# Performance work log

Measured on AMD Instinct MI355X. Metric: run time of the kernel, lower is better.

The kernel has to match this reference:

```python
import jax, jax.numpy as jnp
import numpy as np

N_NODES = 50000
N_EDGES = 400000
IN_CH = 256
HID = 64
OUT_CH = 64
HEADS = 4
N_NTYPES = 3
N_ETYPES = 4
EDGE_DIM = 32
NEG_SLOPE = 0.2
LN_EPS = 1e-5


def _glorot(key, shape, fan_in, fan_out):
    gain = float(np.sqrt(2.0))  # calculate_gain('relu')
    limit = gain * np.sqrt(6.0 / (fan_in + fan_out))
    return jax.random.uniform(key, shape, jnp.float32, -limit, limit)


def setup_inputs() -> dict:
    key = jax.random.key(0)
    ks = jax.random.split(key, 24)
    HC1 = HEADS * HID
    inp = {
        'x': jax.random.normal(ks[0], (N_NODES, IN_CH), jnp.float32),
        'edge_index': jax.random.randint(ks[1], (2, N_EDGES), 0, N_NODES, jnp.int32),
        'node_type': jax.random.randint(ks[2], (N_NODES,), 0, N_NTYPES, jnp.int32),
        'edge_type': jax.random.randint(ks[3], (N_EDGES,), 0, N_ETYPES, jnp.int32),
        'edge_attr': jax.random.normal(ks[4], (N_EDGES, EDGE_DIM), jnp.float32),
        # layer 1 (in -> hid, concat=True)
        'W_src1': _glorot(ks[5], (N_NTYPES, IN_CH, HC1), IN_CH, HC1),
        'W_dst1': _glorot(ks[6], (N_NTYPES, IN_CH, HC1), IN_CH, HC1),
        'att_src1': _glorot(ks[7], (N_ETYPES, HEADS, HID), HEADS, HID),
        'att_dst1': _glorot(ks[8], (N_ETYPES, HEADS, HID), HEADS, HID),
        'W_edge1': _glorot(ks[9], (N_ETYPES, EDGE_DIM, HC1), EDGE_DIM, HC1),
        'att_edge1': _glorot(ks[10], (N_ETYPES, HEADS, HID), HEADS, HID),
        'bias1': jnp.zeros((HC1,), jnp.float32),
        'ln_gamma1': jnp.ones((HC1,), jnp.float32),
        'ln_beta1': jnp.zeros((HC1,), jnp.float32),
        # layer 2 (heads*hid -> out, concat=False)
        'W_src2': _glorot(ks[11], (N_NTYPES, HC1, HEADS * OUT_CH), HC1, HEADS * OUT_CH),
        'W_dst2': _glorot(ks[12], (N_NTYPES, HC1, HEADS * OUT_CH), HC1, HEADS * OUT_CH),
        'att_src2': _glorot(ks[13], (N_ETYPES, HEADS, OUT_CH), HEADS, OUT_CH),
        'att_dst2': _glorot(ks[14], (N_ETYPES, HEADS, OUT_CH), HEADS, OUT_CH),
        'W_edge2': _glorot(ks[15], (N_ETYPES, EDGE_DIM, HEADS * OUT_CH), EDGE_DIM, HEADS * OUT_CH),
        'att_edge2': _glorot(ks[16], (N_ETYPES, HEADS, OUT_CH), HEADS, OUT_CH),
        'bias2': jnp.zeros((OUT_CH,), jnp.float32),
    }
    return inp


def _htgat_conv(x, src, dst, node_type, edge_type, edge_attr,
                W_src, W_dst, att_src, att_dst, W_edge, att_edge, bias, concat):
    N = x.shape[0]
    T_e, H, C = att_src.shape
    # type-specific linear transforms: compute all types, select by node_type
    xs = jnp.einsum('nd,tdo->nto', x, W_src)  # [N, T_n, H*C]
    x_src = jnp.take_along_axis(xs, node_type[:, None, None], axis=1)[:, 0].reshape(N, H, C)
    xd = jnp.einsum('nd,tdo->nto', x, W_dst)
    x_dst = jnp.take_along_axis(xd, node_type[:, None, None], axis=1)[:, 0].reshape(N, H, C)
    # per-(node, edge_type) attention scores, gathered per edge
    s_src = jnp.einsum('nhc,thc->nth', x_src, att_src)  # [N, T_e, H]
    s_dst = jnp.einsum('nhc,thc->nth', x_dst, att_dst)
    et = edge_type[:, None, None]
    alpha = (jnp.take_along_axis(s_src[src], et, axis=1)[:, 0]
             + jnp.take_along_axis(s_dst[dst], et, axis=1)[:, 0])  # [E, H]
    # temporal edge contribution: (edge_attr @ W_edge[t]) . att_edge[t]
    v = jnp.einsum('tdhc,thc->tdh', W_edge.reshape(T_e, -1, H, C), att_edge)
    s_edge = jnp.einsum('ed,tdh->eth', edge_attr, v)  # [E, T_e, H]
    alpha = alpha + jnp.take_along_axis(s_edge, et, axis=1)[:, 0]
    alpha = jnp.where(alpha >= 0, alpha, NEG_SLOPE * alpha)  # leaky_relu
    # segment softmax over destination nodes
    amax = jax.ops.segment_max(alpha, dst, num_segments=N)  # [N, H]
    amax = jnp.where(jnp.isfinite(amax), amax, 0.0)
    ae = jnp.exp(alpha - amax[dst])
    denom = jax.ops.segment_sum(ae, dst, num_segments=N)
    attn = ae / (denom[dst] + 1e-16)  # [E, H]
    # weighted message aggregation (dropout is identity in eval mode)
    msg = x_src[src] * attn[:, :, None]  # [E, H, C]
    out = jax.ops.segment_sum(msg, dst, num_segments=N)  # [N, H, C]
    if concat:
        return out.reshape(N, H * C) + bias
    return out.mean(axis=1) + bias


def _layer_norm(x, gamma, beta):
    mu = x.mean(axis=-1, keepdims=True)
    var = ((x - mu) ** 2).mean(axis=-1, keepdims=True)
    return (x - mu) * jax.lax.rsqrt(var + LN_EPS) * gamma + beta


def reference(x, edge_index, node_type, edge_type, edge_attr,
              W_src1, W_dst1, att_src1, att_dst1, W_edge1, att_edge1, bias1,
              ln_gamma1, ln_beta1,
              W_src2, W_dst2, att_src2, att_dst2, W_edge2, att_edge2, bias2):
    src, dst = edge_index[0], edge_index[1]
    h = _htgat_conv(x, src, dst, node_type, edge_type, edge_attr,
                    W_src1, W_dst1, att_src1, att_dst1, W_edge1, att_edge1, bias1,
                    concat=True)
    h = _layer_norm(h, ln_gamma1, ln_beta1)
    h = jax.nn.elu(h)
    out = _htgat_conv(h, src, dst, node_type, edge_type, edge_attr,
                      W_src2, W_dst2, att_src2, att_dst2, W_edge2, att_edge2, bias2,
                      concat=False)
    return out
```

## Files before the change

kernel.cpp:

```cpp
#include <hip/hip_runtime.h>

#define NN 50000
#define NE 400000
#define NH 4
#define NTY 3
#define ETY 4
#define EDIM 32
#define NBLK 196
#define BM 32

typedef __attribute__((ext_vector_type(8))) short bf16x8;
typedef __attribute__((ext_vector_type(4))) float f32x4;

static __device__ __forceinline__ unsigned short f2bf(float f) {
    unsigned u = __float_as_uint(f);
    unsigned r = (u + 0x7FFFu + ((u >> 16) & 1u)) >> 16;
    return (unsigned short)r;
}
static __device__ __forceinline__ float bf2f(unsigned short s) {
    return __uint_as_float(((unsigned)s) << 16);
}

__global__ __launch_bounds__(256) void prep_fold(
    const float* __restrict__ W_dst1, const float* __restrict__ att_dst1,
    const float* __restrict__ W_edge1, const float* __restrict__ att_edge1,
    const float* __restrict__ W_dst2, const float* __restrict__ att_dst2,
    const float* __restrict__ W_edge2, const float* __restrict__ att_edge2,
    ushort* __restrict__ uf1, ushort* __restrict__ uf2,
    float* __restrict__ v1, float* __restrict__ v2)
{
    int idx = blockIdx.x * 256 + threadIdx.x;
    if (idx < 24576) {
        const float* W; const float* A; ushort* U; int i;
        if (idx < 12288) { W = W_dst1; A = att_dst1; U = uf1; i = idx; }
        else             { W = W_dst2; A = att_dst2; U = uf2; i = idx - 12288; }
        int d = i & 255, h = (i >> 8) & 3, t = (i >> 10) & 3, tn = i >> 12;
        const float* wp = W + tn * 65536 + d * 256 + h * 64;
        const float* ap = A + t * 256 + h * 64;
        float s = 0.f;
        #pragma unroll 8
        for (int c = 0; c < 64; ++c) s += wp[c] * ap[c];
        int th = t * 4 + h;
        int ks = d >> 5, g = (d >> 3) & 3, e = d & 7;
        U[(size_t)tn * 4096 + ks * 512 + (g * 16 + th) * 8 + e] = f2bf(s);
    } else {
        int i = idx - 24576;
        const float* W; const float* A; float* V;
        if (i < 512) { W = W_edge1; A = att_edge1; V = v1; }
        else         { W = W_edge2; A = att_edge2; V = v2; i -= 512; }
        int d = i & 31, h = (i >> 5) & 3, t = i >> 7;
        const float* wp = W + t * (EDIM * 256) + d * 256 + h * 64;
        const float* ap = A + t * 256 + h * 64;
        float s = 0.f;
        #pragma unroll 8
        for (int c = 0; c < 64; ++c) s += wp[c] * ap[c];
        V[(t * 4 + h) * 32 + d] = s;
    }
}

__global__ __launch_bounds__(256) void prep_wt(
    const float* __restrict__ W1, const float* __restrict__ W2,
    ushort* __restrict__ Wf1, ushort* __restrict__ Wf2)
{
    int idx = blockIdx.x * 256 + threadIdx.x;
    const int HALF = 196608;
    const float* W = (idx < HALF) ? W1 : W2;
    ushort* O = (idx < HALF) ? Wf1 : Wf2;
    int i = (idx < HALF) ? idx : idx - HALF;
    int n = i & 255, k = (i >> 8) & 255, t = i >> 16;
    int c16 = n >> 4, r16 = n & 15;
    int ks = k >> 5, g = (k >> 3) & 3, e = k & 7;
    O[(size_t)t * 65536 + (c16 * 8 + ks) * 512 + (g * 16 + r16) * 8 + e] =
        f2bf(W[(size_t)t * 65536 + k * 256 + n]);
}

__global__ void hist_k(const int* __restrict__ dst, int* __restrict__ cnt)
{
    int i = blockIdx.x * 256 + threadIdx.x;
    if (i < NE) atomicAdd(&cnt[dst[i]], 1);
}

__global__ __launch_bounds__(256) void csr_blocksum(
    const int* __restrict__ cnt, const int* __restrict__ ntype,
    int* __restrict__ blks)
{
    int tid = threadIdx.x, b = blockIdx.x;
    int j = b * 256 + tid;
    int c = (j < NN) ? cnt[j] : 0;
    int t = (j < NN) ? ntype[j] : 3;
    int p = (t < 3) ? (1 << (t * 10)) : 0;
    #pragma unroll
    for (int d = 1; d < 64; d <<= 1) { c += __shfl_xor(c, d); p += __shfl_xor(p, d); }
    __shared__ int ws[2][4];
    int lane = tid & 63, w = tid >> 6;
    if (lane == 0) { ws[0][w] = c; ws[1][w] = p; }
    __syncthreads();
    if (tid == 0) {
        int C = ws[0][0] + ws[0][1] + ws[0][2] + ws[0][3];
        int P = ws[1][0] + ws[1][1] + ws[1][2] + ws[1][3];
        blks[b]            = C;
        blks[NBLK + b]     = P & 1023;
        blks[2 * NBLK + b] = (P >> 10) & 1023;
        blks[3 * NBLK + b] = (P >> 20) & 1023;
    }
}

__global__ __launch_bounds__(256) void csr_scanmid(int* __restrict__ blks,
                                                   int* __restrict__ ntoff)
{
    __shared__ int4 part[256];
    int tid = threadIdx.x;
    int4 v = make_int4(0, 0, 0, 0);
    if (tid < NBLK)
        v = make_int4(blks[tid], blks[NBLK + tid], blks[2 * NBLK + tid], blks[3 * NBLK + tid]);
    int4 orig = v;
    part[tid] = v;
    __syncthreads();
    for (int off = 1; off < 256; off <<= 1) {
        int4 u = (tid >= off) ? part[tid - off] : make_int4(0, 0, 0, 0);
        __syncthreads();
        part[tid].x += u.x; part[tid].y += u.y; part[tid].z += u.z; part[tid].w += u.w;
        __syncthreads();
    }
    int4 inc = part[tid];
    if (tid < NBLK) {
        blks[tid]            = inc.x - orig.x;
        blks[NBLK + tid]     = inc.y - orig.y;
        blks[2 * NBLK + tid] = inc.z - orig.z;
        blks[3 * NBLK + tid] = inc.w - orig.w;
    }
    if (tid == 255) {
        ntoff[0] = 0; ntoff[1] = inc.y; ntoff[2] = inc.y + inc.z;
        ntoff[3] = inc.y + inc.z + inc.w;
    }
}

__global__ __launch_bounds__(256) void csr_apply(
    const int* __restrict__ cnt, const int* __restrict__ ntype,
    const int* __restrict__ blks, const int* __restrict__ ntoff,
    int* __restrict__ row_ptr, int* __restrict__ node_perm)
{
    int tid = threadIdx.x, b = blockIdx.x;
    int j = b * 256 + tid;
    int c = (j < NN) ? cnt[j] : 0;
    int t = (j < NN) ? ntype[j] : 3;
    int p = (t < 3) ? (1 << (t * 10)) : 0;
    int lane = tid & 63, w = tid >> 6;
    int ic = c, ip = p;
    #pragma unroll
    for (int d = 1; d < 64; d <<= 1) {
        int uc = __shfl_up(ic, d), up = __shfl_up(ip, d);
        if (lane >= d) { ic += uc; ip += up; }
    }
    __shared__ int ws[2][4];
    if (lane == 63) { ws[0][w] = ic; ws[1][w] = ip; }
    __syncthreads();
    int coff = 0, poff = 0;
    for (int i = 0; i < w; ++i) { coff += ws[0][i]; poff += ws[1][i]; }
    int exc  = ic - c + coff;
    int expp = ip - p + poff;
    if (j < NN) {
        row_ptr[j] = blks[b] + exc;
        if (t < 3) {
            int tb   = blks[(t + 1) * NBLK + b];
            int tpfx = (expp >> (t * 10)) & 1023;
            node_perm[ntoff[t] + tb + tpfx] = j;
        }
    }
    if (j == 0) row_ptr[NN] = NE;
}

__global__ void scatter_k(const int* __restrict__ src, const int* __restrict__ dst,
                          const int* __restrict__ etype,
                          const int* __restrict__ row_ptr, int* __restrict__ cursor,
                          int* __restrict__ perm, int* __restrict__ spk)
{
    int i = blockIdx.x * 256 + threadIdx.x;
    if (i < NE) {
        int d = dst[i];
        int pos = row_ptr[d] + atomicAdd(&cursor[d], 1);
        perm[pos] = i;
        spk[pos] = src[i] | (etype[i] << 16);
    }
}

__global__ __launch_bounds__(256) void gemm3_k(
    const ushort* __restrict__ xb, const float* __restrict__ xf,
    const ushort* __restrict__ Wf, const ushort* __restrict__ Uf,
    const float* __restrict__ att_src,
    const int* __restrict__ node_perm, const int* __restrict__ ntoff,
    ushort* __restrict__ xout, float* __restrict__ s_dst,
    float* __restrict__ s_src)
{
    int t = blockIdx.z;
    int seg0 = ntoff[t], seg1 = ntoff[t + 1];
    int row0 = seg0 + blockIdx.x * BM;
    if (row0 >= seg1) return;

    __shared__ __align__(16) ushort Xl[BM * 256];

    int tid = threadIdx.x;
    int w = tid >> 6, l = tid & 63;
    int kb = (tid & 31) * 16;

    #pragma unroll
    for (int it = 0; it < 4; ++it) {
        int row = it * 8 + (tid >> 5);
        int rp = row0 + row;
        int gr = (rp < seg1) ? node_perm[rp] : 0;
        uint4 pv;
        if (xf) {
            const char* src = (const char*)(xf + (size_t)gr * 256) + kb * 2;
            float4 f0 = *(const float4*)(src);
            float4 f1 = *(const float4*)(src + 16);
            pv.x = (unsigned)f2bf(f0.x) | ((unsigned)f2bf(f0.y) << 16);
            pv.y = (unsigned)f2bf(f0.z) | ((unsigned)f2bf(f0.w) << 16);
            pv.z = (unsigned)f2bf(f1.x) | ((unsigned)f2bf(f1.y) << 16);
            pv.w = (unsigned)f2bf(f1.z) | ((unsigned)f2bf(f1.w) << 16);
        } else {
            pv = *(const uint4*)((const char*)(xb + (size_t)gr * 256) + kb);
        }
        *(uint4*)((char*)Xl + row * 512 + (kb ^ ((row & 7) << 4))) = pv;
    }
    __syncthreads();

    int g = l >> 4, r16 = l & 15;
    const ushort* wfb = Wf + (size_t)(t * 16 + w * 4) * 8 * 512;
    const ushort* ufb = Uf + (size_t)t * 4096;

    f32x4 acc[2][4];
    #pragma unroll
    for (int i = 0; i < 2; ++i)
        #pragma unroll
        for (int j = 0; j < 4; ++j) acc[i][j] = (f32x4){0.f, 0.f, 0.f, 0.f};
    f32x4 uacc[2] = {{0.f,0.f,0.f,0.f},{0.f,0.f,0.f,0.f}};

    #pragma unroll
    for (int ks = 0; ks < 8; ++ks) {
        int kbyte = ks * 64 + g * 16;
        bf16x8 b0 = *(const bf16x8*)((const char*)Xl + r16 * 512 + (kbyte ^ ((r16 & 7) << 4)));
        bf16x8 b1 = *(const bf16x8*)((const char*)Xl + (16 + r16) * 512 + (kbyte ^ (((16 + r16) & 7) << 4)));
        #pragma unroll
        for (int cf = 0; cf < 4; ++cf) {
            bf16x8 a = *(const bf16x8*)(wfb + (cf * 8 + ks) * 512 + l * 8);
            acc[0][cf] = __builtin_amdgcn_mfma_f32_16x16x32_bf16(a, b0, acc[0][cf], 0, 0, 0);
            acc[1][cf] = __builtin_amdgcn_mfma_f32_16x16x32_bf16(a, b1, acc[1][cf], 0, 0, 0);
        }
        bf16x8 ua = *(const bf16x8*)(ufb + ks * 512 + l * 8);
        uacc[0] = __builtin_amdgcn_mfma_f32_16x16x32_bf16(ua, b0, uacc[0], 0, 0, 0);
        uacc[1] = __builtin_amdgcn_mfma_f32_16x16x32_bf16(ua, b1, uacc[1], 0, 0, 0);
    }

    float p[4][2];
    #pragma unroll
    for (int te = 0; te < 4; ++te) { p[te][0] = 0.f; p[te][1] = 0.f; }
    #pragma unroll
    for (int te = 0; te < 4; ++te) {
        #pragma unroll
        for (int cf = 0; cf < 4; ++cf) {
            float4 av = *(const float4*)(att_src + te * 256 + w * 64 + cf * 16 + g * 4);
            #pragma unroll
            for (int fr = 0; fr < 2; ++fr) {
                p[te][fr] += acc[fr][cf][0] * av.x + acc[fr][cf][1] * av.y
                           + acc[fr][cf][2] * av.z + acc[fr][cf][3] * av.w;
            }
        }
    }
    #pragma unroll
    for (int te = 0; te < 4; ++te)
        #pragma unroll
        for (int fr = 0; fr < 2; ++fr) {
            p[te][fr] += __shfl_xor(p[te][fr], 16);
            p[te][fr] += __shfl_xor(p[te][fr], 32);
        }

    int col0 = w * 64;
    #pragma unroll
    for (int fr = 0; fr < 2; ++fr) {
        int rp = row0 + fr * 16 + r16;
        if (rp < seg1) {
            int gr = node_perm[rp];
            ushort* orow = xout + (size_t)gr * 256;
            #pragma unroll
            for (int cf = 0; cf < 4; ++cf) {
                ushort4 o;
                o.x = f2bf(acc[fr][cf][0]); o.y = f2bf(acc[fr][cf][1]);
                o.z = f2bf(acc[fr][cf][2]); o.w = f2bf(acc[fr][cf][3]);
                *(ushort4*)(orow + col0 + cf * 16 + g * 4) = o;
            }
            if (w == 0) {
                *(float4*)(s_dst + (size_t)gr * 16 + g * 4) =
                    make_float4(uacc[fr][0], uacc[fr][1], uacc[fr][2], uacc[fr][3]);
            }
            if (g == 0) {
                #pragma unroll
                for (int te = 0; te < 4; ++te)
                    s_src[(size_t)gr * 16 + te * 4 + w] = p[te][fr];
            }
        }
    }
}

__global__ void sedge2_k(const float* __restrict__ eattr,
                         const int* __restrict__ perm, const int* __restrict__ spk,
                         const float* __restrict__ v1, const float* __restrict__ v2,
                         float* __restrict__ sedge1c, float* __restrict__ sedge2c)
{
    int k = blockIdx.x * 256 + threadIdx.x;
    if (k >= NE) return;
    int e = perm[k];
    int t = spk[k] >> 16;
    float4 ea[8];
    #pragma unroll
    for (int i = 0; i < 8; ++i) ea[i] = *(const float4*)(eattr + (size_t)e * 32 + i * 4);
    float4 o1, o2;
    #pragma unroll
    for (int h = 0; h < 4; ++h) {
        const float* vp1 = v1 + (t * 4 + h) * 32;
        const float* vp2 = v2 + (t * 4 + h) * 32;
        float s1 = 0.f, s2 = 0.f;
        #pragma unroll
        for (int i = 0; i < 8; ++i) {
            float4 w1 = *(const float4*)(vp1 + i * 4);
            float4 w2 = *(const float4*)(vp2 + i * 4);
            s1 += ea[i].x * w1.x + ea[i].y * w1.y + ea[i].z * w1.z + ea[i].w * w1.w;
            s2 += ea[i].x * w2.x + ea[i].y * w2.y + ea[i].z * w2.z + ea[i].w * w2.w;
        }
        ((float*)&o1)[h] = s1;
        ((float*)&o2)[h] = s2;
    }
    *(float4*)(sedge1c + (size_t)k * 4) = o1;
    *(float4*)(sedge2c + (size_t)k * 4) = o2;
}

static __device__ __forceinline__ float4 alpha_slot(
    int k, int n, const int* __restrict__ spk, const float* __restrict__ s_src,
    const float* __restrict__ s_dst, const float* __restrict__ sedgec, int* sOut)
{
    int pk = spk[k];
    int s = pk & 0xFFFF;
    int t = pk >> 16;
    float4 ss = *(const float4*)(s_src + (size_t)s * 16 + t * 4);
    float4 sd = *(const float4*)(s_dst + (size_t)n * 16 + t * 4);
    float4 se = *(const float4*)(sedgec + (size_t)k * 4);
    float4 a;
    a.x = ss.x + sd.x + se.x; a.x = (a.x >= 0.f) ? a.x : 0.2f * a.x;
    a.y = ss.y + sd.y + se.y; a.y = (a.y >= 0.f) ? a.y : 0.2f * a.y;
    a.z = ss.z + sd.z + se.z; a.z = (a.z >= 0.f) ? a.z : 0.2f * a.z;
    a.w = ss.w + sd.w + se.w; a.w = (a.w >= 0.f) ? a.w : 0.2f * a.w;
    *sOut = s;
    return a;
}

__global__ __launch_bounds__(256) void attn_k(
    const ushort* __restrict__ xsb, const float* __restrict__ s_src,
    const float* __restrict__ s_dst, const float* __restrict__ sedgec,
    const int* __restrict__ row_ptr, const int* __restrict__ spk,
    const float* __restrict__ bias, const float* __restrict__ gamma,
    const float* __restrict__ beta, void* __restrict__ out, int mode)
{
    __shared__ float  wlds[16][256];
    __shared__ int    slds[16][64];
    __shared__ float4 mxl[16], invl[16];

    int w = threadIdx.x >> 6;
    int lane = threadIdx.x & 63;
    int j = lane >> 4, li = lane & 15;
    int nid = w * 4 + j;
    int n = blockIdx.x * 16 + nid;
    int beg = row_ptr[n], end = row_ptr[n + 1];
    int deg = end - beg;

    int k0 = beg + li;
    bool act = li < deg;
    int sF = 0;
    float4 aF = make_float4(-1e30f, -1e30f, -1e30f, -1e30f);
    if (act) aF = alpha_slot(k0, n, spk, s_src, s_dst, sedgec, &sF);

    float4 mx = aF;
    for (int k = k0 + 16; k < end; k += 16) {
        int s2; float4 t = alpha_slot(k, n, spk, s_src, s_dst, sedgec, &s2);
        mx.x = fmaxf(mx.x, t.x); mx.y = fmaxf(mx.y, t.y);
        mx.z = fmaxf(mx.z, t.z); mx.w = fmaxf(mx.w, t.w);
    }
    #pragma unroll
    for (int d = 1; d < 16; d <<= 1) {
        mx.x = fmaxf(mx.x, __shfl_xor(mx.x, d, 16));
        mx.y = fmaxf(mx.y, __shfl_xor(mx.y, d, 16));
        mx.z = fmaxf(mx.z, __shfl_xor(mx.z, d, 16));
        mx.w = fmaxf(mx.w, __shfl_xor(mx.w, d, 16));
    }
    float4 ex = make_float4(0.f, 0.f, 0.f, 0.f);
    if (act) {
        ex.x = __expf(aF.x - mx.x); ex.y = __expf(aF.y - mx.y);
        ex.z = __expf(aF.z - mx.z); ex.w = __expf(aF.w - mx.w);
    }
    float4 sm = ex;
    for (int k = k0 + 16; k < end; k += 16) {
        int s2; float4 t = alpha_slot(k, n, spk, s_src, s_dst, sedgec, &s2);
        sm.x += __expf(t.x - mx.x); sm.y += __expf(t.y - mx.y);
        sm.z += __expf(t.z - mx.z); sm.w += __expf(t.w - mx.w);
    }
    #pragma unroll
    for (int d = 1; d < 16; d <<= 1) {
        sm.x += __shfl_xor(sm.x, d, 16); sm.y += __shfl_xor(sm.y, d, 16);
        sm.z += __shfl_xor(sm.z, d, 16); sm.w += __shfl_xor(sm.w, d, 16);
    }
    float4 inv;
    inv.x = 1.f / (sm.x + 1e-16f); inv.y = 1.f / (sm.y + 1e-16f);
    inv.z = 1.f / (sm.z + 1e-16f); inv.w = 1.f / (sm.w + 1e-16f);

    if (act) {
        *(float4*)&wlds[nid][li * 4] = make_float4(ex.x * inv.x, ex.y * inv.y,
                                                   ex.z * inv.z, ex.w * inv.w);
        slds[nid][li] = sF;
    }
    for (int k = k0 + 16; k < end && (k - beg) < 64; k += 16) {
        int s2; float4 t = alpha_slot(k, n, spk, s_src, s_dst, sedgec, &s2);
        int slot = k - beg;
        *(float4*)&wlds[nid][slot * 4] = make_float4(
            __expf(t.x - mx.x) * inv.x, __expf(t.y - mx.y) * inv.y,
            __expf(t.z - mx.z) * inv.z, __expf(t.w - mx.w) * inv.w);
        slds[nid][slot] = s2;
    }
    if (li == 0) { mxl[nid] = mx; invl[nid] = inv; }

    int h2 = lane >> 4;
    for (int jj = 0; jj < 4; ++jj) {
        int nb = w * 4 + jj;
        int nn = blockIdx.x * 16 + nb;
        int begj = __shfl(beg, jj * 16);
        int degj = __shfl(deg, jj * 16);

        float4 acc = make_float4(0.f, 0.f, 0.f, 0.f);
        int nfast = (degj < 64) ? degj : 64;
        for (int i = 0; i < nfast; ++i) {
            float wv = wlds[nb][i * 4 + h2];
            int s = slds[nb][i];
            ushort4 xv = *(const ushort4*)(xsb + (size_t)s * 256 + lane * 4);
            acc.x += wv * bf2f(xv.x);
            acc.y += wv * bf2f(xv.y);
            acc.z += wv * bf2f(xv.z);
            acc.w += wv * bf2f(xv.w);
        }
        if (degj > 64) {
            float4 mxj = mxl[nb], invj = invl[nb];
            float mxh  = (h2 == 0) ? mxj.x  : (h2 == 1) ? mxj.y  : (h2 == 2) ? mxj.z  : mxj.w;
            float invh = (h2 == 0) ? invj.x : (h2 == 1) ? invj.y : (h2 == 2) ? invj.z : invj.w;
            for (int k = begj + 64; k < begj + degj; ++k) {
                int pk = spk[k];
                int s = pk & 0xFFFF, t = pk >> 16;
                float a = s_src[(size_t)s * 16 + t * 4 + h2]
                        + s_dst[(size_t)nn * 16 + t * 4 + h2]
                        + sedgec[(size_t)k * 4 + h2];
                a = (a >= 0.f) ? a : 0.2f * a;
                float wv = __expf(a - mxh) * invh;
                ushort4 xv = *(const ushort4*)(xsb + (size_t)s * 256 + lane * 4);
                acc.x += wv * bf2f(xv.x);
                acc.y += wv * bf2f(xv.y);
                acc.z += wv * bf2f(xv.z);
                acc.w += wv * bf2f(xv.w);
            }
        }

        if (mode == 1) {
            float4 bb = *(const float4*)(bias + lane * 4);
            float vals[4] = { acc.x + bb.x, acc.y + bb.y, acc.z + bb.z, acc.w + bb.w };
            float s = vals[0] + vals[1] + vals[2] + vals[3];
            s += __shfl_xor(s, 1); s += __shfl_xor(s, 2); s += __shfl_xor(s, 4);
            s += __shfl_xor(s, 8); s += __shfl_xor(s, 16); s += __shfl_xor(s, 32);
            float mu = s * (1.f / 256.f);
            float q = 0.f;
            #pragma unroll
            for (int jq = 0; jq < 4; ++jq) { float d = vals[jq] - mu; q += d * d; }
            q += __shfl_xor(q, 1); q += __shfl_xor(q, 2); q += __shfl_xor(q, 4);
            q += __shfl_xor(q, 8); q += __shfl_xor(q, 16); q += __shfl_xor(q, 32);
            float r = rsqrtf(q * (1.f / 256.f) + 1e-5f);
            float4 gg = *(const float4*)(gamma + lane * 4);
            float4 be = *(const float4*)(beta + lane * 4);
            ushort4 o; float y;
            y = (vals[0] - mu) * r * gg.x + be.x; o.x = f2bf((y > 0.f) ? y : (__expf(y) - 1.f));
            y = (vals[1] - mu) * r * gg.y + be.y; o.y = f2bf((y > 0.f) ? y : (__expf(y) - 1.f));
            y = (vals[2] - mu) * r * gg.z + be.z; o.z = f2bf((y > 0.f) ? y : (__expf(y) - 1.f));
            y = (vals[3] - mu) * r * gg.w + be.w; o.w = f2bf((y > 0.f) ? y : (__expf(y) - 1.f));
            *(ushort4*)((ushort*)out + (size_t)nn * 256 + lane * 4) = o;
        } else {
            float4 am = acc;
            am.x += __shfl_xor(am.x, 16); am.x += __shfl_xor(am.x, 32);
            am.y += __shfl_xor(am.y, 16); am.y += __shfl_xor(am.y, 32);
            am.z += __shfl_xor(am.z, 16); am.z += __shfl_xor(am.z, 32);
            am.w += __shfl_xor(am.w, 16); am.w += __shfl_xor(am.w, 32);
            if (lane < 16) {
                float4 bb = *(const float4*)(bias + lane * 4);
                float4 o;
                o.x = am.x * 0.25f + bb.x;
                o.y = am.y * 0.25f + bb.y;
                o.z = am.z * 0.25f + bb.z;
                o.w = am.w * 0.25f + bb.w;
                *(float4*)((float*)out + (size_t)nn * 64 + lane * 4) = o;
            }
        }
    }
}

extern "C" void kernel_launch(void* const* d_in, const int* in_sizes, int n_in,
                              void* d_out, int out_size, void* d_ws, size_t ws_size,
                              hipStream_t stream)
{
    (void)in_sizes; (void)n_in; (void)out_size;
    const float* x        = (const float*)d_in[0];
    const int*   ei       = (const int*)d_in[1];
    const int*   ntype    = (const int*)d_in[2];
    const int*   etype    = (const int*)d_in[3];
    const float* eattr    = (const float*)d_in[4];
    const float* W_src1   = (const float*)d_in[5];
    const float* W_dst1   = (const float*)d_in[6];
    const float* att_src1 = (const float*)d_in[7];
    const float* att_dst1 = (const float*)d_in[8];
    const float* W_edge1  = (const float*)d_in[9];
    const float* att_edge1= (const float*)d_in[10];
    const float* bias1    = (const float*)d_in[11];
    const float* gamma1   = (const float*)d_in[12];
    const float* beta1    = (const float*)d_in[13];
    const float* W_src2   = (const float*)d_in[14];
    const float* W_dst2   = (const float*)d_in[15];
    const float* att_src2 = (const float*)d_in[16];
    const float* att_dst2 = (const float*)d_in[17];
    const float* W_edge2  = (const float*)d_in[18];
    const float* att_edge2= (const float*)d_in[19];
    const float* bias2    = (const float*)d_in[20];

    char* w = (char*)d_ws;
    size_t off = 0;
    auto carve = [&](size_t bytes) -> char* {
        char* p = w + off;
        off = (off + bytes + 255) & ~(size_t)255;
        return p;
    };
    ushort* x_srcb  = (ushort*)carve((size_t)NN * 256 * 2);
    ushort* hb      = (ushort*)carve((size_t)NN * 256 * 2);
    float* s_src    = (float*)carve((size_t)NN * 16 * 4);
    float* s_dst    = (float*)carve((size_t)NN * 16 * 4);
    float* sedge1c  = (float*)carve((size_t)NE * 4 * 4);
    float* sedge2c  = (float*)carve((size_t)NE * 4 * 4);
    int*   cnt      = (int*)carve((size_t)(2 * NN) * 4);
    int*   cursor   = cnt + NN;
    int*   row_ptr  = (int*)carve((size_t)(NN + 1) * 4);
    int*   perm     = (int*)carve((size_t)NE * 4);
    int*   spk      = (int*)carve((size_t)NE * 4);
    int*   node_perm= (int*)carve((size_t)NN * 4);
    int*   ntoff    = (int*)carve(4 * 4);
    int*   blks     = (int*)carve((size_t)(4 * NBLK) * 4);
    ushort* uf1     = (ushort*)carve(12288 * 2);
    ushort* uf2     = (ushort*)carve(12288 * 2);
    float* v1       = (float*)carve(512 * 4);
    float* v2       = (float*)carve(512 * 4);
    ushort* Wf1     = (ushort*)carve((size_t)196608 * 2);
    ushort* Wf2     = (ushort*)carve((size_t)196608 * 2);
    if (off > ws_size) return;

    const int* srca = ei;
    const int* dsta = ei + NE;

    hipMemsetAsync(cnt, 0, (size_t)(2 * NN) * 4, stream);

    prep_fold<<<100, 256, 0, stream>>>(W_dst1, att_dst1, W_edge1, att_edge1,
                                       W_dst2, att_dst2, W_edge2, att_edge2,
                                       uf1, uf2, v1, v2);
    prep_wt<<<1536, 256, 0, stream>>>(W_src1, W_src2, Wf1, Wf2);
    hist_k<<<(NE + 255) / 256, 256, 0, stream>>>(dsta, cnt);
    csr_blocksum<<<NBLK, 256, 0, stream>>>(cnt, ntype, blks);
    csr_scanmid<<<1, 256, 0, stream>>>(blks, ntoff);
    csr_apply<<<NBLK, 256, 0, stream>>>(cnt, ntype, blks, ntoff, row_ptr, node_perm);
    scatter_k<<<(NE + 255) / 256, 256, 0, stream>>>(srca, dsta, etype, row_ptr,
                                                    cursor, perm, spk);
    sedge2_k<<<(NE + 255) / 256, 256, 0, stream>>>(eattr, perm, spk, v1, v2,
                                                   sedge1c, sedge2c);

    dim3 ggrid((NN + BM - 1) / BM, 1, NTY);

    gemm3_k<<<ggrid, 256, 0, stream>>>(nullptr, x, Wf1, uf1, att_src1,
                                       node_perm, ntoff, x_srcb, s_dst, s_src);
    attn_k<<<NN / 16, 256, 0, stream>>>(x_srcb, s_src, s_dst, sedge1c, row_ptr, spk,
                                        bias1, gamma1, beta1, hb, 1);

    gemm3_k<<<ggrid, 256, 0, stream>>>(hb, nullptr, Wf2, uf2, att_src2,
                                       node_perm, ntoff, x_srcb, s_dst, s_src);
    attn_k<<<NN / 16, 256, 0, stream>>>(x_srcb, s_src, s_dst, sedge2c, row_ptr, spk,
                                        bias2, nullptr, nullptr, d_out, 2);
}
```

Baseline: 278.5 us.

## Fuse edge-score projection into scatter, compact GEMM grid, prefetch weight fragments

The edge-attribute score projection now runs inside scatter_k and writes directly to the CSR-ordered position. This removes the separate sedge2_k kernel along with the perm array and its indirect reads. The node-type GEMM now uses a flat 1-D grid whose per-type block offsets are computed in csr_scanmid, so roughly two thirds of the launched blocks no longer exit immediately. The GEMM k-loop also double-buffers the weight fragment loads one step ahead of the MFMAs. The price is higher register pressure in the GEMM and uncoalesced scattered float4 stores of the edge scores.

```diff
diff --git a/kernel.cpp b/kernel.cpp
--- a/kernel.cpp
+++ b/kernel.cpp
@@ -8,6 +8,7 @@
 #define EDIM 32
 #define NBLK 196
 #define BM 32
+#define GGRID ((NN + BM - 1) / BM + NTY)
 
 typedef __attribute__((ext_vector_type(8))) short bf16x8;
 typedef __attribute__((ext_vector_type(4))) float f32x4;
@@ -106,7 +107,8 @@
 }
 
 __global__ __launch_bounds__(256) void csr_scanmid(int* __restrict__ blks,
-                                                   int* __restrict__ ntoff)
+                                                   int* __restrict__ ntoff,
+                                                   int* __restrict__ gblk)
 {
     __shared__ int4 part[256];
     int tid = threadIdx.x;
@@ -132,6 +134,10 @@
     if (tid == 255) {
         ntoff[0] = 0; ntoff[1] = inc.y; ntoff[2] = inc.y + inc.z;
         ntoff[3] = inc.y + inc.z + inc.w;
+        int b0 = (inc.y + BM - 1) / BM;
+        int b1 = (inc.z + BM - 1) / BM;
+        int b2 = (inc.w + BM - 1) / BM;
+        gblk[0] = 0; gblk[1] = b0; gblk[2] = b0 + b1; gblk[3] = b0 + b1 + b2;
     }
 }
 
@@ -170,18 +176,42 @@
     if (j == 0) row_ptr[NN] = NE;
 }
 
-__global__ void scatter_k(const int* __restrict__ src, const int* __restrict__ dst,
-                          const int* __restrict__ etype,
-                          const int* __restrict__ row_ptr, int* __restrict__ cursor,
-                          int* __restrict__ perm, int* __restrict__ spk)
+__global__ __launch_bounds__(256) void scatter_k(
+    const int* __restrict__ src, const int* __restrict__ dst,
+    const int* __restrict__ etype, const float* __restrict__ eattr,
+    const float* __restrict__ v1, const float* __restrict__ v2,
+    const int* __restrict__ row_ptr, int* __restrict__ cursor,
+    int* __restrict__ spk,
+    float* __restrict__ sedge1c, float* __restrict__ sedge2c)
 {
     int i = blockIdx.x * 256 + threadIdx.x;
-    if (i < NE) {
-        int d = dst[i];
-        int pos = row_ptr[d] + atomicAdd(&cursor[d], 1);
-        perm[pos] = i;
-        spk[pos] = src[i] | (etype[i] << 16);
-    }
+    if (i >= NE) return;
+    int d = dst[i];
+    int pos = row_ptr[d] + atomicAdd(&cursor[d], 1);
+    int t = etype[i];
+    spk[pos] = src[i] | (t << 16);
+
+    float4 ea[8];
+    #pragma unroll
+    for (int q = 0; q < 8; ++q) ea[q] = *(const float4*)(eattr + (size_t)i * 32 + q * 4);
+    float4 o1, o2;
+    #pragma unroll
+    for (int h = 0; h < 4; ++h) {
+        const float* vp1 = v1 + (t * 4 + h) * 32;
+        const float* vp2 = v2 + (t * 4 + h) * 32;
+        float s1 = 0.f, s2 = 0.f;
+        #pragma unroll
+        for (int q = 0; q < 8; ++q) {
+            float4 w1 = *(const float4*)(vp1 + q * 4);
+            float4 w2 = *(const float4*)(vp2 + q * 4);
+            s1 += ea[q].x * w1.x + ea[q].y * w1.y + ea[q].z * w1.z + ea[q].w * w1.w;
+            s2 += ea[q].x * w2.x + ea[q].y * w2.y + ea[q].z * w2.z + ea[q].w * w2.w;
+        }
+        ((float*)&o1)[h] = s1;
+        ((float*)&o2)[h] = s2;
+    }
+    *(float4*)(sedge1c + (size_t)pos * 4) = o1;
+    *(float4*)(sedge2c + (size_t)pos * 4) = o2;
 }
 
 __global__ __launch_bounds__(256) void gemm3_k(
@@ -189,13 +219,15 @@
     const ushort* __restrict__ Wf, const ushort* __restrict__ Uf,
     const float* __restrict__ att_src,
     const int* __restrict__ node_perm, const int* __restrict__ ntoff,
+    const int* __restrict__ gblk,
     ushort* __restrict__ xout, float* __restrict__ s_dst,
     float* __restrict__ s_src)
 {
-    int t = blockIdx.z;
-    int seg0 = ntoff[t], seg1 = ntoff[t + 1];
-    int row0 = seg0 + blockIdx.x * BM;
-    if (row0 >= seg1) return;
+    int b = blockIdx.x;
+    if (b >= gblk[3]) return;
+    int t = (b >= gblk[1]) + (b >= gblk[2]);
+    int row0 = ntoff[t] + (b - gblk[t]) * BM;
+    int seg1 = ntoff[t + 1];
 
     __shared__ __align__(16) ushort Xl[BM * 256];
 
@@ -235,20 +267,35 @@
         for (int j = 0; j < 4; ++j) acc[i][j] = (f32x4){0.f, 0.f, 0.f, 0.f};
     f32x4 uacc[2] = {{0.f,0.f,0.f,0.f},{0.f,0.f,0.f,0.f}};
 
+    bf16x8 aW[4], aU, nW[4], nU;
+    #pragma unroll
+    for (int cf = 0; cf < 4; ++cf)
+        aW[cf] = *(const bf16x8*)(wfb + (cf * 8 + 0) * 512 + l * 8);
+    aU = *(const bf16x8*)(ufb + 0 * 512 + l * 8);
+
     #pragma unroll
     for (int ks = 0; ks < 8; ++ks) {
+        if (ks < 7) {
+            #pragma unroll
+            for (int cf = 0; cf < 4; ++cf)
+                nW[cf] = *(const bf16x8*)(wfb + (cf * 8 + ks + 1) * 512 + l * 8);
+            nU = *(const bf16x8*)(ufb + (ks + 1) * 512 + l * 8);
+        }
         int kbyte = ks * 64 + g * 16;
         bf16x8 b0 = *(const bf16x8*)((const char*)Xl + r16 * 512 + (kbyte ^ ((r16 & 7) << 4)));
         bf16x8 b1 = *(const bf16x8*)((const char*)Xl + (16 + r16) * 512 + (kbyte ^ (((16 + r16) & 7) << 4)));
         #pragma unroll
         for (int cf = 0; cf < 4; ++cf) {
-            bf16x8 a = *(const bf16x8*)(wfb + (cf * 8 + ks) * 512 + l * 8);
-            acc[0][cf] = __builtin_amdgcn_mfma_f32_16x16x32_bf16(a, b0, acc[0][cf], 0, 0, 0);
-            acc[1][cf] = __builtin_amdgcn_mfma_f32_16x16x32_bf16(a, b1, acc[1][cf], 0, 0, 0);
-        }
-        bf16x8 ua = *(const bf16x8*)(ufb + ks * 512 + l * 8);
-        uacc[0] = __builtin_amdgcn_mfma_f32_16x16x32_bf16(ua, b0, uacc[0], 0, 0, 0);
-        uacc[1] = __builtin_amdgcn_mfma_f32_16x16x32_bf16(ua, b1, uacc[1], 0, 0, 0);
+            acc[0][cf] = __builtin_amdgcn_mfma_f32_16x16x32_bf16(aW[cf], b0, acc[0][cf], 0, 0, 0);
+            acc[1][cf] = __builtin_amdgcn_mfma_f32_16x16x32_bf16(aW[cf], b1, acc[1][cf], 0, 0, 0);
+        }
+        uacc[0] = __builtin_amdgcn_mfma_f32_16x16x32_bf16(aU, b0, uacc[0], 0, 0, 0);
+        uacc[1] = __builtin_amdgcn_mfma_f32_16x16x32_bf16(aU, b1, uacc[1], 0, 0, 0);
+        if (ks < 7) {
+            #pragma unroll
+            for (int cf = 0; cf < 4; ++cf) aW[cf] = nW[cf];
+            aU = nU;
+        }
     }
 
     float p[4][2];
@@ -299,38 +346,6 @@
             }
         }
     }
-}
-
-__global__ void sedge2_k(const float* __restrict__ eattr,
-                         const int* __restrict__ perm, const int* __restrict__ spk,
-                         const float* __restrict__ v1, const float* __restrict__ v2,
-                         float* __restrict__ sedge1c, float* __restrict__ sedge2c)
-{
-    int k = blockIdx.x * 256 + threadIdx.x;
-    if (k >= NE) return;
-    int e = perm[k];
-    int t = spk[k] >> 16;
-    float4 ea[8];
-    #pragma unroll
-    for (int i = 0; i < 8; ++i) ea[i] = *(const float4*)(eattr + (size_t)e * 32 + i * 4);
-    float4 o1, o2;
-    #pragma unroll
-    for (int h = 0; h < 4; ++h) {
-        const float* vp1 = v1 + (t * 4 + h) * 32;
-        const float* vp2 = v2 + (t * 4 + h) * 32;
-        float s1 = 0.f, s2 = 0.f;
-        #pragma unroll
-        for (int i = 0; i < 8; ++i) {
-            float4 w1 = *(const float4*)(vp1 + i * 4);
-            float4 w2 = *(const float4*)(vp2 + i * 4);
-            s1 += ea[i].x * w1.x + ea[i].y * w1.y + ea[i].z * w1.z + ea[i].w * w1.w;
-            s2 += ea[i].x * w2.x + ea[i].y * w2.y + ea[i].z * w2.z + ea[i].w * w2.w;
-        }
-        ((float*)&o1)[h] = s1;
-        ((float*)&o2)[h] = s2;
-    }
-    *(float4*)(sedge1c + (size_t)k * 4) = o1;
-    *(float4*)(sedge2c + (size_t)k * 4) = o2;
 }
 
 static __device__ __forceinline__ float4 alpha_slot(
@@ -546,10 +561,10 @@
     int*   cnt      = (int*)carve((size_t)(2 * NN) * 4);
     int*   cursor   = cnt + NN;
     int*   row_ptr  = (int*)carve((size_t)(NN + 1) * 4);
-    int*   perm     = (int*)carve((size_t)NE * 4);
     int*   spk      = (int*)carve((size_t)NE * 4);
     int*   node_perm= (int*)carve((size_t)NN * 4);
     int*   ntoff    = (int*)carve(4 * 4);
+    int*   gblk     = (int*)carve(4 * 4);
     int*   blks     = (int*)carve((size_t)(4 * NBLK) * 4);
     ushort* uf1     = (ushort*)carve(12288 * 2);
     ushort* uf2     = (ushort*)carve(12288 * 2);
@@ -570,22 +585,19 @@
     prep_wt<<<1536, 256, 0, stream>>>(W_src1, W_src2, Wf1, Wf2);
     hist_k<<<(NE + 255) / 256, 256, 0, stream>>>(dsta, cnt);
     csr_blocksum<<<NBLK, 256, 0, stream>>>(cnt, ntype, blks);
-    csr_scanmid<<<1, 256, 0, stream>>>(blks, ntoff);
+    csr_scanmid<<<1, 256, 0, stream>>>(blks, ntoff, gblk);
     csr_apply<<<NBLK, 256, 0, stream>>>(cnt, ntype, blks, ntoff, row_ptr, node_perm);
-    scatter_k<<<(NE + 255) / 256, 256, 0, stream>>>(srca, dsta, etype, row_ptr,
-                                                    cursor, perm, spk);
-    sedge2_k<<<(NE + 255) / 256, 256, 0, stream>>>(eattr, perm, spk, v1, v2,
-                                                   sedge1c, sedge2c);
-
-    dim3 ggrid((NN + BM - 1) / BM, 1, NTY);
-
-    gemm3_k<<<ggrid, 256, 0, stream>>>(nullptr, x, Wf1, uf1, att_src1,
-                                       node_perm, ntoff, x_srcb, s_dst, s_src);
+    scatter_k<<<(NE + 255) / 256, 256, 0, stream>>>(srca, dsta, etype, eattr, v1, v2,
+                                                    row_ptr, cursor, spk,
+                                                    sedge1c, sedge2c);
+
+    gemm3_k<<<GGRID, 256, 0, stream>>>(nullptr, x, Wf1, uf1, att_src1,
+                                       node_perm, ntoff, gblk, x_srcb, s_dst, s_src);
     attn_k<<<NN / 16, 256, 0, stream>>>(x_srcb, s_src, s_dst, sedge1c, row_ptr, spk,
                                         bias1, gamma1, beta1, hb, 1);
 
-    gemm3_k<<<ggrid, 256, 0, stream>>>(hb, nullptr, Wf2, uf2, att_src2,
-                                       node_perm, ntoff, x_srcb, s_dst, s_src);
+    gemm3_k<<<GGRID, 256, 0, stream>>>(hb, nullptr, Wf2, uf2, att_src2,
+                                       node_perm, ntoff, gblk, x_srcb, s_dst, s_src);
     attn_k<<<NN / 16, 256, 0, stream>>>(x_srcb, s_src, s_dst, sedge2c, row_ptr, spk,
                                         bias2, nullptr, nullptr, d_out, 2);
 }
```

Result: faster. 254.8 us (-8.5%).
